# Kernel tuning notes

Hardware: AMD Instinct MI355X
Metric: run time of the kernel (lower is better)

Reference implementation:

```python
import jax, jax.numpy as jnp
import numpy as np

B, A, N_IN, N_HID, N_OUT, MAX_Z = 2048, 96, 128, 64, 1, 100
SHIFT = float(np.log(2.0))

def ssp(x):
    # shifted softplus: softplus(x) - log(2)
    return jax.nn.softplus(x) - SHIFT

def setup_inputs() -> dict:
    key = jax.random.key(0)
    ks = jax.random.split(key, 8)
    rep = jax.random.normal(ks[0], (B, A, N_IN), dtype=jnp.float32)
    atomic_numbers = jax.random.randint(ks[1], (B, A), 0, MAX_Z)
    atom_mask = jnp.ones((B, A), dtype=jnp.float32)
    s1 = 1.0 / np.sqrt(N_IN)
    s2 = 1.0 / np.sqrt(N_HID)
    W1 = jax.random.uniform(ks[2], (N_IN, N_HID), jnp.float32, -s1, s1)
    b1 = jax.random.uniform(ks[3], (N_HID,), jnp.float32, -s1, s1)
    W2 = jax.random.uniform(ks[4], (N_HID, N_OUT), jnp.float32, -s2, s2)
    b2 = jax.random.uniform(ks[5], (N_OUT,), jnp.float32, -s2, s2)
    atomref_table = jax.random.normal(ks[6], (MAX_Z, N_OUT), dtype=jnp.float32) * 0.1
    atomref_table = atomref_table.at[0].set(0.0)  # mask-atom reference is zero
    mean = jnp.array([0.0], dtype=jnp.float32)
    stddev = jnp.array([1.0], dtype=jnp.float32)
    return {"representation": rep, "atomic_numbers": atomic_numbers,
            "atom_mask": atom_mask, "W1": W1, "b1": b1, "W2": W2, "b2": b2,
            "atomref_table": atomref_table, "mean": mean, "stddev": stddev}

def reference(representation, atomic_numbers, atom_mask, W1, b1, W2, b2,
              atomref_table, mean, stddev):
    # per-atom MLP: [B,A,n_in] -> [B,A,n_out]
    h = ssp(jnp.einsum('bai,ih->bah', representation, W1) + b1)
    yi = jnp.einsum('bah,ho->bao', h, W2) + b2
    # standardize (ScaleShift): y * stddev + mean
    yi = yi * stddev + mean
    # atomref embedding lookup and add
    yi = yi + atomref_table[atomic_numbers]  # [B,A,n_out]
    # masked sum aggregation over atoms (Aggregate axis=1, mean=False)
    y = jnp.sum(yi * atom_mask[..., None], axis=1)  # [B,n_out]
    return y
```

## Files before the change

kernel.cpp:

```cpp
#include <hip/hip_runtime.h>

#define BB 2048
#define AA 96
#define NIN 128
#define NHID 64
#define MI 4

typedef __attribute__((ext_vector_type(8))) short bf16x8;
typedef __attribute__((ext_vector_type(4))) float f32x4;

static __device__ __forceinline__ unsigned f2bf(float x) {
    unsigned u = __builtin_bit_cast(unsigned, x);
    return (u + 0x7FFFu + ((u >> 16) & 1u)) >> 16;
}
static __device__ __forceinline__ unsigned cvt_pk_bf16(float a, float b) {
    return f2bf(a) | (f2bf(b) << 16);
}

__global__ __launch_bounds__(256, 4) void atomwise_kernel(
    const float* __restrict__ rep,
    const int*   __restrict__ zs,
    const float* __restrict__ mask,
    const float* __restrict__ w1,
    const float* __restrict__ b1,
    const float* __restrict__ w2,
    const float* __restrict__ b2,
    const float* __restrict__ aref,
    const float* __restrict__ mean,
    const float* __restrict__ stddev,
    float* __restrict__ out)
{
    const int lane = threadIdx.x & 63;
    const int wv   = threadIdx.x >> 6;
    const int nl   = lane & 15;
    const int quad = lane >> 4;
    const int wave_atom0 = (blockIdx.x * 4 + wv) * (16 * MI);

    bf16x8 bq[4][4];
    #pragma unroll
    for (int s = 0; s < 4; ++s) {
        #pragma unroll
        for (int t = 0; t < 4; ++t) {
            union { bf16x8 v; unsigned u[4]; } fb;
            #pragma unroll
            for (int jp = 0; jp < 4; ++jp) {
                const int k = s * 32 + quad * 8 + jp * 2;
                const int n = t * 16 + nl;
                fb.u[jp] = cvt_pk_bf16(w1[k * NHID + n], w1[(k + 1) * NHID + n]);
            }
            bq[s][t] = fb.v;
        }
    }
    float b1v[4], w2v[4];
    #pragma unroll
    for (int t = 0; t < 4; ++t) { b1v[t] = b1[t * 16 + nl]; w2v[t] = w2[t * 16 + nl]; }
    const float sdv  = stddev[0];
    const float cadd = fmaf(b2[0], sdv, mean[0]);

    const float LOG2E = 1.4426950408889634f;
    const float LN2   = 0.6931471805599453f;

    #pragma unroll 1
    for (int mt = 0; mt < MI; ++mt) {
        const int atom0 = wave_atom0 + mt * 16;
        const float* rowp = rep + (size_t)(atom0 + nl) * NIN + quad * 8;

        float4 q[4][2];
        #pragma unroll
        for (int s = 0; s < 4; ++s) {
            q[s][0] = *reinterpret_cast<const float4*>(rowp + s * 32);
            q[s][1] = *reinterpret_cast<const float4*>(rowp + s * 32 + 4);
        }

        f32x4 acc[4];
        #pragma unroll
        for (int t = 0; t < 4; ++t) acc[t] = (f32x4){0.f, 0.f, 0.f, 0.f};

        #pragma unroll
        for (int s = 0; s < 4; ++s) {
            union { bf16x8 v; unsigned u[4]; } fa;
            fa.u[0] = cvt_pk_bf16(q[s][0].x, q[s][0].y);
            fa.u[1] = cvt_pk_bf16(q[s][0].z, q[s][0].w);
            fa.u[2] = cvt_pk_bf16(q[s][1].x, q[s][1].y);
            fa.u[3] = cvt_pk_bf16(q[s][1].z, q[s][1].w);
            #pragma unroll
            for (int t = 0; t < 4; ++t)
                acc[t] = __builtin_amdgcn_mfma_f32_16x16x32_bf16(fa.v, bq[s][t], acc[t], 0, 0, 0);
        }

        float v[4];
        #pragma unroll
        for (int r = 0; r < 4; ++r) {
            float p = 0.f;
            #pragma unroll
            for (int t = 0; t < 4; ++t) {
                float x  = acc[t][r] + b1v[t];
                float ax = fabsf(x);
                float em = exp2f(-ax * LOG2E);
                float sp = fmaxf(x, 0.f) + log2f(1.f + em) * LN2;
                p = fmaf(sp - LN2, w2v[t], p);
            }
            p += __shfl_xor(p, 1); p += __shfl_xor(p, 2);
            p += __shfl_xor(p, 4); p += __shfl_xor(p, 8);
            v[r] = p;
        }
        if (nl == 0) {
            #pragma unroll
            for (int r = 0; r < 4; ++r) {
                const int ag = atom0 + quad * 4 + r;
                const float yi = fmaf(v[r], sdv, cadd) + aref[zs[ag]];
                atomicAdd(out + ag / AA, mask[ag] * yi);
            }
        }
    }
}

extern "C" void kernel_launch(void* const* d_in, const int* in_sizes, int n_in,
                              void* d_out, int out_size, void* d_ws, size_t ws_size,
                              hipStream_t stream) {
    const float* rep    = (const float*)d_in[0];
    const int*   zs     = (const int*)  d_in[1];
    const float* mask   = (const float*)d_in[2];
    const float* w1     = (const float*)d_in[3];
    const float* b1     = (const float*)d_in[4];
    const float* w2     = (const float*)d_in[5];
    const float* b2     = (const float*)d_in[6];
    const float* aref   = (const float*)d_in[7];
    const float* mean   = (const float*)d_in[8];
    const float* stddev = (const float*)d_in[9];
    float* out = (float*)d_out;

    (void)hipMemsetAsync(out, 0, (size_t)out_size * sizeof(float), stream);

    const int atoms  = BB * AA;
    const int blocks = atoms / (4 * 16 * MI);
    atomwise_kernel<<<dim3(blocks), dim3(256), 0, stream>>>(
        rep, zs, mask, w1, b1, w2, b2, aref, mean, stddev, out);
}
```

Baseline: 188.6 us.

## Stage transposed W1 in LDS, prefetch next tile, and reduce atomics per wave

Each block now converts W1 to bf16 once into a padded, transposed shared-memory buffer, replacing the per-lane strided global gather that built the B fragments in registers. The representation load for the next 16-atom tile is issued before the current tile's MFMAs, so global latency overlaps compute. Per-atom atomicAdds become one shuffle-reduced atomic per 16-atom tile. MI drops from 4 to 3, giving more blocks. The cost is LDS traffic for B fragments on every tile plus a block-wide sync at the start.

```diff
diff --git a/kernel.cpp b/kernel.cpp
--- a/kernel.cpp
+++ b/kernel.cpp
@@ -4,7 +4,8 @@
 #define AA 96
 #define NIN 128
 #define NHID 64
-#define MI 4
+#define MI 3
+#define WST 136
 
 typedef __attribute__((ext_vector_type(8))) short bf16x8;
 typedef __attribute__((ext_vector_type(4))) float f32x4;
@@ -13,7 +14,7 @@
     unsigned u = __builtin_bit_cast(unsigned, x);
     return (u + 0x7FFFu + ((u >> 16) & 1u)) >> 16;
 }
-static __device__ __forceinline__ unsigned cvt_pk_bf16(float a, float b) {
+static __device__ __forceinline__ unsigned cvt_pk(float a, float b) {
     return f2bf(a) | (f2bf(b) << 16);
 }
 
@@ -30,46 +31,70 @@
     const float* __restrict__ stddev,
     float* __restrict__ out)
 {
-    const int lane = threadIdx.x & 63;
-    const int wv   = threadIdx.x >> 6;
+    __shared__ unsigned short w1t[NHID * WST];
+
+    const int tid  = threadIdx.x;
+    const int lane = tid & 63;
+    const int wv   = tid >> 6;
     const int nl   = lane & 15;
     const int quad = lane >> 4;
-    const int wave_atom0 = (blockIdx.x * 4 + wv) * (16 * MI);
 
-    bf16x8 bq[4][4];
-    #pragma unroll
-    for (int s = 0; s < 4; ++s) {
+    {
+        const float4* w14 = (const float4*)w1;
         #pragma unroll
-        for (int t = 0; t < 4; ++t) {
-            union { bf16x8 v; unsigned u[4]; } fb;
-            #pragma unroll
-            for (int jp = 0; jp < 4; ++jp) {
-                const int k = s * 32 + quad * 8 + jp * 2;
-                const int n = t * 16 + nl;
-                fb.u[jp] = cvt_pk_bf16(w1[k * NHID + n], w1[(k + 1) * NHID + n]);
-            }
-            bq[s][t] = fb.v;
+        for (int i = 0; i < 8; ++i) {
+            const int    idx = tid + i * 256;
+            const float4 v   = w14[idx];
+            const int e = idx * 4;
+            const int k = e >> 6, n = e & 63;
+            w1t[(n    ) * WST + k] = (unsigned short)f2bf(v.x);
+            w1t[(n + 1) * WST + k] = (unsigned short)f2bf(v.y);
+            w1t[(n + 2) * WST + k] = (unsigned short)f2bf(v.z);
+            w1t[(n + 3) * WST + k] = (unsigned short)f2bf(v.w);
         }
     }
+    __syncthreads();
+
     float b1v[4], w2v[4];
     #pragma unroll
     for (int t = 0; t < 4; ++t) { b1v[t] = b1[t * 16 + nl]; w2v[t] = w2[t * 16 + nl]; }
     const float sdv  = stddev[0];
     const float cadd = fmaf(b2[0], sdv, mean[0]);
 
+    const int wave_atom0 = (blockIdx.x * 4 + wv) * (16 * MI);
+
     const float LOG2E = 1.4426950408889634f;
     const float LN2   = 0.6931471805599453f;
+
+    float4 q[8];
+    {
+        const float* rowp = rep + (size_t)(wave_atom0 + nl) * NIN + quad * 8;
+        #pragma unroll
+        for (int s = 0; s < 4; ++s) {
+            q[2 * s]     = *(const float4*)(rowp + s * 32);
+            q[2 * s + 1] = *(const float4*)(rowp + s * 32 + 4);
+        }
+    }
 
     #pragma unroll 1
     for (int mt = 0; mt < MI; ++mt) {
         const int atom0 = wave_atom0 + mt * 16;
-        const float* rowp = rep + (size_t)(atom0 + nl) * NIN + quad * 8;
 
-        float4 q[4][2];
+        union { bf16x8 v; unsigned u[4]; } fa[4];
         #pragma unroll
         for (int s = 0; s < 4; ++s) {
-            q[s][0] = *reinterpret_cast<const float4*>(rowp + s * 32);
-            q[s][1] = *reinterpret_cast<const float4*>(rowp + s * 32 + 4);
+            fa[s].u[0] = cvt_pk(q[2 * s].x,     q[2 * s].y);
+            fa[s].u[1] = cvt_pk(q[2 * s].z,     q[2 * s].w);
+            fa[s].u[2] = cvt_pk(q[2 * s + 1].x, q[2 * s + 1].y);
+            fa[s].u[3] = cvt_pk(q[2 * s + 1].z, q[2 * s + 1].w);
+        }
+        if (mt + 1 < MI) {
+            const float* rowp = rep + (size_t)(atom0 + 16 + nl) * NIN + quad * 8;
+            #pragma unroll
+            for (int s = 0; s < 4; ++s) {
+                q[2 * s]     = *(const float4*)(rowp + s * 32);
+                q[2 * s + 1] = *(const float4*)(rowp + s * 32 + 4);
+            }
         }
 
         f32x4 acc[4];
@@ -78,14 +103,12 @@
 
         #pragma unroll
         for (int s = 0; s < 4; ++s) {
-            union { bf16x8 v; unsigned u[4]; } fa;
-            fa.u[0] = cvt_pk_bf16(q[s][0].x, q[s][0].y);
-            fa.u[1] = cvt_pk_bf16(q[s][0].z, q[s][0].w);
-            fa.u[2] = cvt_pk_bf16(q[s][1].x, q[s][1].y);
-            fa.u[3] = cvt_pk_bf16(q[s][1].z, q[s][1].w);
+            const int k0 = s * 32 + quad * 8;
             #pragma unroll
-            for (int t = 0; t < 4; ++t)
-                acc[t] = __builtin_amdgcn_mfma_f32_16x16x32_bf16(fa.v, bq[s][t], acc[t], 0, 0, 0);
+            for (int t = 0; t < 4; ++t) {
+                const bf16x8 bf = *(const bf16x8*)&w1t[(t * 16 + nl) * WST + k0];
+                acc[t] = __builtin_amdgcn_mfma_f32_16x16x32_bf16(fa[s].v, bf, acc[t], 0, 0, 0);
+            }
         }
 
         float v[4];
@@ -105,12 +128,16 @@
             v[r] = p;
         }
         if (nl == 0) {
+            float ssum = 0.f;
             #pragma unroll
             for (int r = 0; r < 4; ++r) {
                 const int ag = atom0 + quad * 4 + r;
                 const float yi = fmaf(v[r], sdv, cadd) + aref[zs[ag]];
-                atomicAdd(out + ag / AA, mask[ag] * yi);
+                ssum += mask[ag] * yi;
             }
+            ssum += __shfl_xor(ssum, 16);
+            ssum += __shfl_xor(ssum, 32);
+            if (lane == 0) atomicAdd(out + atom0 / AA, ssum);
         }
     }
 }
```

Measured after the change: 187.1 us. Within noise of the previous version (-0.8%).

## Stage W1 fragments in LDS and pre-reduce atomics per 16-atom tile

Applied to the files above, without the earlier changes.

Each block now converts W1 into bf16 MFMA fragments once, stores them in shared memory, and keeps b1 and w2 there too. Before, every wave built its own register copy of the weights. Per-atom atomicAdds are replaced by a cross-quad shuffle reduction, so each 16-atom tile issues one atomic to its molecule's output. The tile count per wave drops from 4 to 3, the min-blocks launch bound is removed, and the rep loads move inside a non-unrolled k-loop. That last change lowers register pressure but cuts how many loads are in flight at once.

```diff
diff --git a/kernel.cpp b/kernel.cpp
--- a/kernel.cpp
+++ b/kernel.cpp
@@ -4,7 +4,7 @@
 #define AA 96
 #define NIN 128
 #define NHID 64
-#define MI 4
+#define MI 3
 
 typedef __attribute__((ext_vector_type(8))) short bf16x8;
 typedef __attribute__((ext_vector_type(4))) float f32x4;
@@ -13,11 +13,11 @@
     unsigned u = __builtin_bit_cast(unsigned, x);
     return (u + 0x7FFFu + ((u >> 16) & 1u)) >> 16;
 }
-static __device__ __forceinline__ unsigned cvt_pk_bf16(float a, float b) {
+static __device__ __forceinline__ unsigned cvt_pk(float a, float b) {
     return f2bf(a) | (f2bf(b) << 16);
 }
 
-__global__ __launch_bounds__(256, 4) void atomwise_kernel(
+__global__ __launch_bounds__(256) void atomwise_kernel(
     const float* __restrict__ rep,
     const int*   __restrict__ zs,
     const float* __restrict__ mask,
@@ -30,62 +30,61 @@
     const float* __restrict__ stddev,
     float* __restrict__ out)
 {
-    const int lane = threadIdx.x & 63;
-    const int wv   = threadIdx.x >> 6;
+    __shared__ bf16x8 w1f[1024];
+    __shared__ float  b1s[NHID], w2s[NHID];
+
+    const int tid  = threadIdx.x;
+    const int lane = tid & 63;
+    const int wv   = tid >> 6;
     const int nl   = lane & 15;
     const int quad = lane >> 4;
-    const int wave_atom0 = (blockIdx.x * 4 + wv) * (16 * MI);
 
-    bf16x8 bq[4][4];
     #pragma unroll
-    for (int s = 0; s < 4; ++s) {
+    for (int f = 0; f < 4; ++f) {
+        const int fid = tid + f * 256;
+        const int l2  = fid & 63;
+        const int st  = fid >> 6;
+        const int k0  = (st >> 2) * 32 + (l2 >> 4) * 8;
+        const int n   = (st & 3) * 16 + (l2 & 15);
+        union { bf16x8 v; unsigned u[4]; } fb;
         #pragma unroll
-        for (int t = 0; t < 4; ++t) {
-            union { bf16x8 v; unsigned u[4]; } fb;
-            #pragma unroll
-            for (int jp = 0; jp < 4; ++jp) {
-                const int k = s * 32 + quad * 8 + jp * 2;
-                const int n = t * 16 + nl;
-                fb.u[jp] = cvt_pk_bf16(w1[k * NHID + n], w1[(k + 1) * NHID + n]);
-            }
-            bq[s][t] = fb.v;
-        }
+        for (int jp = 0; jp < 4; ++jp)
+            fb.u[jp] = cvt_pk(w1[(k0 + 2 * jp) * NHID + n],
+                              w1[(k0 + 2 * jp + 1) * NHID + n]);
+        w1f[fid] = fb.v;
     }
-    float b1v[4], w2v[4];
-    #pragma unroll
-    for (int t = 0; t < 4; ++t) { b1v[t] = b1[t * 16 + nl]; w2v[t] = w2[t * 16 + nl]; }
+    if (tid < NHID) { b1s[tid] = b1[tid]; w2s[tid] = w2[tid]; }
+    __syncthreads();
+
     const float sdv  = stddev[0];
     const float cadd = fmaf(b2[0], sdv, mean[0]);
-
     const float LOG2E = 1.4426950408889634f;
     const float LN2   = 0.6931471805599453f;
 
+    const int wid = blockIdx.x * 4 + wv;
+
     #pragma unroll 1
     for (int mt = 0; mt < MI; ++mt) {
-        const int atom0 = wave_atom0 + mt * 16;
+        const int atom0 = (wid * MI + mt) * 16;
         const float* rowp = rep + (size_t)(atom0 + nl) * NIN + quad * 8;
-
-        float4 q[4][2];
-        #pragma unroll
-        for (int s = 0; s < 4; ++s) {
-            q[s][0] = *reinterpret_cast<const float4*>(rowp + s * 32);
-            q[s][1] = *reinterpret_cast<const float4*>(rowp + s * 32 + 4);
-        }
 
         f32x4 acc[4];
         #pragma unroll
         for (int t = 0; t < 4; ++t) acc[t] = (f32x4){0.f, 0.f, 0.f, 0.f};
 
-        #pragma unroll
+        #pragma unroll 1
         for (int s = 0; s < 4; ++s) {
+            const float4 a0 = *(const float4*)(rowp + s * 32);
+            const float4 a1 = *(const float4*)(rowp + s * 32 + 4);
             union { bf16x8 v; unsigned u[4]; } fa;
-            fa.u[0] = cvt_pk_bf16(q[s][0].x, q[s][0].y);
-            fa.u[1] = cvt_pk_bf16(q[s][0].z, q[s][0].w);
-            fa.u[2] = cvt_pk_bf16(q[s][1].x, q[s][1].y);
-            fa.u[3] = cvt_pk_bf16(q[s][1].z, q[s][1].w);
+            fa.u[0] = cvt_pk(a0.x, a0.y);
+            fa.u[1] = cvt_pk(a0.z, a0.w);
+            fa.u[2] = cvt_pk(a1.x, a1.y);
+            fa.u[3] = cvt_pk(a1.z, a1.w);
+            const bf16x8* fr = &w1f[s * 256 + lane];
             #pragma unroll
             for (int t = 0; t < 4; ++t)
-                acc[t] = __builtin_amdgcn_mfma_f32_16x16x32_bf16(fa.v, bq[s][t], acc[t], 0, 0, 0);
+                acc[t] = __builtin_amdgcn_mfma_f32_16x16x32_bf16(fa.v, fr[t * 64], acc[t], 0, 0, 0);
         }
 
         float v[4];
@@ -94,23 +93,27 @@
             float p = 0.f;
             #pragma unroll
             for (int t = 0; t < 4; ++t) {
-                float x  = acc[t][r] + b1v[t];
+                float x  = acc[t][r] + b1s[t * 16 + nl];
                 float ax = fabsf(x);
                 float em = exp2f(-ax * LOG2E);
                 float sp = fmaxf(x, 0.f) + log2f(1.f + em) * LN2;
-                p = fmaf(sp - LN2, w2v[t], p);
+                p = fmaf(sp - LN2, w2s[t * 16 + nl], p);
             }
             p += __shfl_xor(p, 1); p += __shfl_xor(p, 2);
             p += __shfl_xor(p, 4); p += __shfl_xor(p, 8);
             v[r] = p;
         }
         if (nl == 0) {
+            float ssum = 0.f;
             #pragma unroll
             for (int r = 0; r < 4; ++r) {
                 const int ag = atom0 + quad * 4 + r;
                 const float yi = fmaf(v[r], sdv, cadd) + aref[zs[ag]];
-                atomicAdd(out + ag / AA, mask[ag] * yi);
+                ssum += mask[ag] * yi;
             }
+            ssum += __shfl_xor(ssum, 16);
+            ssum += __shfl_xor(ssum, 32);
+            if (lane == 0) atomicAdd(out + atom0 / AA, ssum);
         }
     }
 }
```

New measurement: 166.1 us. 1.14x faster.
